# Kernel tuning notes

Measured on AMD Instinct MI355X. Metric: run time of the kernel, lower is better.

Reference implementation:

```python
import jax, jax.numpy as jnp
import numpy as np

N1 = 6000
N2 = 6000
H = 256
F_DIM = 768
G_DIM = 64
KNN = 5


def setup_inputs() -> dict:
    key = jax.random.key(0)
    ks = jax.random.split(key, 12)
    d = {
        "src_feature_0": jax.random.normal(ks[0], (N1, F_DIM), jnp.float32),
        "src_feature_1": jax.random.normal(ks[1], (N2, F_DIM), jnp.float32),
        "src_embedding_0": jax.random.normal(ks[2], (N1, H), jnp.float32),
        "src_embedding_1": jax.random.normal(ks[3], (N2, H), jnp.float32),
        "src_y_0": jax.random.randint(ks[4], (N1,), 0, 2, jnp.int64),
        "src_y_1": jax.random.randint(ks[5], (N2,), 0, 2, jnp.int64),
        "src_graphlet_0": jax.random.normal(ks[6], (N1, G_DIM), jnp.float32),
        "src_graphlet_1": jax.random.normal(ks[7], (N2, G_DIM), jnp.float32),
        # GCNConv params: lin weight [out,in] (applied as x @ W.T), bias [out]
        "gnn_weight": jax.random.normal(ks[8], (H, H), jnp.float32) / np.sqrt(H),
        "gnn_bias": jnp.zeros((H,), jnp.float32),
        # Attention combiner: Linear(H, 1)
        "attn_weight": jax.random.normal(ks[9], (1, H), jnp.float32) / np.sqrt(H),
        "attn_bias": jnp.zeros((1,), jnp.float32),
    }
    return d


def _construct_edges(emb, n_list, knn):
    """kNN cross-domain graph: cosine sim, zero within-domain blocks, row-wise topk.
    Returns (src, dst, edge_weight_indicator) with exactly N*knn candidate edges;
    edges whose masked similarity is exactly 0 get weight 0 (mirrors torch.nonzero
    dropping them)."""
    n = emb.shape[0]
    v = emb / jnp.maximum(jnp.linalg.norm(emb, axis=1, keepdims=True), 1e-12)
    adj = v @ v.T  # [N, N] dense similarity
    # zero the within-domain diagonal blocks
    dom_id = jnp.concatenate([jnp.full((m,), i, jnp.int32) for i, m in enumerate(n_list)])
    same = dom_id[:, None] == dom_id[None, :]
    adj = jnp.where(same, 0.0, adj)
    topk_val, topk_idx = jax.lax.top_k(adj, knn)  # [N, knn]
    src = jnp.repeat(jnp.arange(n, dtype=jnp.int32), knn)      # sp_row
    dst = topk_idx.reshape(-1).astype(jnp.int32)                # sp_col
    w = (topk_val.reshape(-1) != 0.0).astype(emb.dtype)         # existing-edge indicator
    return src, dst, w


def _gcn(x, src, dst, w, weight, bias):
    """PyG GCNConv with add_self_loops and symmetric normalization."""
    n = x.shape[0]
    loop = jnp.arange(n, dtype=jnp.int32)
    s = jnp.concatenate([src, loop])
    t = jnp.concatenate([dst, loop])
    ew = jnp.concatenate([w, jnp.ones((n,), x.dtype)])
    deg = jax.ops.segment_sum(ew, t, num_segments=n)
    dinv = jnp.where(deg > 0, jax.lax.rsqrt(jnp.maximum(deg, 1e-30)), 0.0)
    norm = dinv[s] * ew * dinv[t]  # [E]
    xw = x @ weight.T              # [N, H]
    msg = norm[:, None] * xw[s]    # gather + scale
    out = jax.ops.segment_sum(msg, t, num_segments=n)  # scatter-add at targets
    return out + bias


def _attention(inputs, w, b):
    stacked = jnp.stack(inputs, axis=1)                 # [N, 2, H]
    scores = stacked @ w.T + b                          # [N, 2, 1]
    weights = jax.nn.softmax(scores, axis=1)
    return jnp.sum(stacked * weights, axis=1)           # [N, H]


def _simple_mmd(x, y):
    # linear-kernel MMD: squared distance of mean embeddings
    d = jnp.mean(x, axis=0) - jnp.mean(y, axis=0)
    return jnp.sum(d * d)


def reference(src_feature_0, src_feature_1, src_embedding_0, src_embedding_1,
              src_y_0, src_y_1, src_graphlet_0, src_graphlet_1,
              gnn_weight, gnn_bias, attn_weight, attn_bias):
    n_list = [src_feature_0.shape[0], src_feature_1.shape[0]]
    emb = jnp.concatenate([src_embedding_0, src_embedding_1], axis=0)  # [N, H]
    # graph construction is under torch.no_grad
    src, dst, w = _construct_edges(jax.lax.stop_gradient(emb), n_list, KNN)
    updated = _gcn(emb, src, dst, w, gnn_weight, gnn_bias)
    updated = _attention([emb, updated], attn_weight, attn_bias)  # cross_output == 'concat'
    # src_pair_loss: pairwise MMD over domains, i != j, halved
    e0 = updated[:n_list[0]]
    e1 = updated[n_list[0]:]
    loss = (_simple_mmd(e0, e1) + _simple_mmd(e1, e0)) / 2.0
    return loss, updated
```

## Files before the change

kernel.cpp:

```cpp
#include <hip/hip_runtime.h>
#include <stdint.h>

typedef unsigned short u16;
typedef __attribute__((ext_vector_type(8))) short bf16x8;
typedef __attribute__((ext_vector_type(4))) float f32x4;
typedef __attribute__((ext_vector_type(4))) unsigned short us4;

#define ND 6000
#define NT 12000
#define HD 256
#define NCH 8
#define CHW 750
#define LDH 136

__device__ __forceinline__ float bf2f(unsigned int u) {
  u = (u & 0xffffu) << 16;
  return __builtin_bit_cast(float, u);
}
__device__ __forceinline__ u16 f2bf(float f) {
  unsigned int x = __builtin_bit_cast(unsigned int, f);
  x += 0x7fffu + ((x >> 16) & 1u);
  return (u16)(x >> 16);
}
template <int M>
__device__ __forceinline__ void tk_ins(float x, int idx, float* tv, int* ti) {
  #pragma unroll
  for (int k = 0; k < M; ++k) {
    if (x > tv[k]) { float ov = tv[k]; int oi = ti[k]; tv[k] = x; ti[k] = idx; x = ov; idx = oi; }
  }
}

__global__ __launch_bounds__(256) void k_prep(const void* __restrict__ e0, const void* __restrict__ e1,
                                              const void* __restrict__ gw, const void* __restrict__ gb,
                                              const void* __restrict__ aw, const void* __restrict__ ab,
                                              u16* __restrict__ ce, u16* __restrict__ cgwh,
                                              float* __restrict__ pgb, float* __restrict__ paw,
                                              float* __restrict__ pab, float* __restrict__ rinv,
                                              double* __restrict__ rinv64,
                                              int* __restrict__ cnt, int* __restrict__ fill,
                                              float* __restrict__ macc, int* __restrict__ flag) {
  const int b = blockIdx.x, tid = threadIdx.x;
  uint2 du = ((const uint2*)e0)[tid];
  float dv0 = bf2f(du.x), dv2 = bf2f(du.y);
  int big = (!(fabsf(dv0) <= 1024.0f)) || (!(fabsf(dv2) <= 1024.0f));
  const int isf32 = __syncthreads_or(big);
  if (b == 0 && tid == 0) flag[0] = isf32;

  if (b < 3000) {
    int i = b * 256 + tid;
    const void* src; int li;
    if (i < 384000) { src = e0; li = i; } else { src = e1; li = i - 384000; }
    us4 h;
    float f0, f1, f2, f3;
    if (isf32) {
      float4 v = ((const float4*)src)[li];
      f0 = v.x; f1 = v.y; f2 = v.z; f3 = v.w;
      h[0] = f2bf(v.x); h[1] = f2bf(v.y); h[2] = f2bf(v.z); h[3] = f2bf(v.w);
    } else {
      h = ((const us4*)src)[li];
      f0 = bf2f(h[0]); f1 = bf2f(h[1]); f2 = bf2f(h[2]); f3 = bf2f(h[3]);
    }
    *(us4*)(ce + (size_t)i * 4) = h;
    double s = (double)f0 * f0 + (double)f1 * f1 + (double)f2 * f2 + (double)f3 * f3;
    #pragma unroll
    for (int off = 32; off > 0; off >>= 1) s += __shfl_xor(s, off);
    if ((tid & 63) == 0) {
      double rd = 1.0 / fmax(sqrt(s), 1e-12);
      int node = i >> 6;
      rinv[node] = (float)rd;
      rinv64[node] = rd;
    }
    if (b < 47) {
      int k = b * 256 + tid;
      if (k < NT) { cnt[k] = 0; fill[k] = 0; }
      if (k < 512) macc[k] = 0.0f;
    }
  } else if (b < 3064) {
    int i = (b - 3000) * 256 + tid;
    us4 h;
    if (isf32) {
      float4 v = ((const float4*)gw)[i];
      h[0] = f2bf(v.x); h[1] = f2bf(v.y); h[2] = f2bf(v.z); h[3] = f2bf(v.w);
    } else {
      h = ((const us4*)gw)[i];
    }
    *(us4*)(cgwh + (size_t)i * 4) = h;
  } else {
    if (isf32) {
      pgb[tid] = ((const float*)gb)[tid];
      paw[tid] = ((const float*)aw)[tid];
      if (tid == 0) pab[0] = ((const float*)ab)[0];
    } else {
      pgb[tid] = bf2f(((const u16*)gb)[tid]);
      paw[tid] = bf2f(((const u16*)aw)[tid]);
      if (tid == 0) pab[0] = bf2f(((const u16*)ab)[0]);
    }
  }
}

__global__ __launch_bounds__(256) void k_sim(const u16* __restrict__ ce, const float* __restrict__ rinv,
                                             float* __restrict__ pval, int* __restrict__ pidx) {
  const int pass = blockIdx.z;
  const int qrow0 = pass ? ND : 0;
  const int crow0 = pass ? 0 : ND;
  const int qbase = blockIdx.x * 64;
  const int cch = blockIdx.y * CHW;
  const int cend = (cch + CHW < ND) ? cch + CHW : ND;
  const int tid = threadIdx.x, w = tid >> 6, l = tid & 63;
  const int l15 = l & 15, lq = l >> 4;

  __shared__ __align__(16) short ldsC[64 * LDH];

  int ql = qbase + w * 16 + l15; if (ql > ND - 1) ql = ND - 1;
  const u16* qh = ce + (size_t)(qrow0 + ql) * HD;
  bf16x8 afh[8];
  #pragma unroll
  for (int kk = 0; kk < 8; ++kk) afh[kk] = *(const bf16x8*)(qh + kk * 32 + lq * 8);
  const u16* C = ce + (size_t)crow0 * HD;

  unsigned int tvl[4][8];
  #pragma unroll
  for (int j = 0; j < 4; ++j)
    #pragma unroll
    for (int k = 0; k < 8; ++k) tvl[j][k] = 0u;

  for (int c0 = cch; c0 < cend; c0 += 64) {
    f32x4 acc[4];
    #pragma unroll
    for (int ct = 0; ct < 4; ++ct) acc[ct] = (f32x4){0.f, 0.f, 0.f, 0.f};
    #pragma unroll
    for (int kh = 0; kh < 2; ++kh) {
      #pragma unroll
      for (int sw = 0; sw < 4; ++sw) {
        int flat = (sw * 256 + tid) * 8;
        int r = flat >> 7, col = flat & 127;
        int cr = c0 + r; if (cr > cend - 1) cr = cend - 1;
        *(int4*)&ldsC[r * LDH + col] = *(const int4*)(C + (size_t)cr * HD + kh * 128 + col);
      }
      __syncthreads();
      #pragma unroll
      for (int ks = 0; ks < 4; ++ks) {
        #pragma unroll
        for (int ct = 0; ct < 4; ++ct) {
          bf16x8 bh = *(const bf16x8*)&ldsC[(ct * 16 + l15) * LDH + ks * 32 + lq * 8];
          acc[ct] = __builtin_amdgcn_mfma_f32_16x16x32_bf16(bh, afh[kh * 4 + ks], acc[ct], 0, 0, 0);
        }
      }
      __syncthreads();
    }
    const float* rbase = rinv + crow0 + c0 + lq * 4;
    const int lim = cend - c0;
    const int cl0 = (c0 - cch) + lq * 4;
    if (lim >= 64) {
      #pragma unroll
      for (int ct = 0; ct < 4; ++ct) {
        float4 rc = *(const float4*)(rbase + ct * 16);
        float rcv[4] = {rc.x, rc.y, rc.z, rc.w};
        #pragma unroll
        for (int r = 0; r < 4; ++r) {
          float x = acc[ct][r] * rcv[r];
          unsigned int u = __builtin_bit_cast(unsigned int, x);
          unsigned int ord = u ^ ((unsigned int)((int)u >> 31) | 0x80000000u);
          unsigned int key = (ord & 0xFFFFFC00u) | (unsigned int)(cl0 + ct * 16 + r);
          #pragma unroll
          for (int k = 0; k < 8; ++k) {
            unsigned int hi = key > tvl[r][k] ? key : tvl[r][k];
            key = key > tvl[r][k] ? tvl[r][k] : key;
            tvl[r][k] = hi;
          }
        }
      }
    } else {
      #pragma unroll
      for (int ct = 0; ct < 4; ++ct) {
        float4 rc = *(const float4*)(rbase + ct * 16);
        float rcv[4] = {rc.x, rc.y, rc.z, rc.w};
        #pragma unroll
        for (int r = 0; r < 4; ++r) {
          int cl64 = ct * 16 + lq * 4 + r;
          float x = acc[ct][r] * rcv[r];
          unsigned int u = __builtin_bit_cast(unsigned int, x);
          unsigned int ord = u ^ ((unsigned int)((int)u >> 31) | 0x80000000u);
          unsigned int key = (cl64 < lim)
              ? ((ord & 0xFFFFFC00u) | (unsigned int)(cl0 + ct * 16 + r)) : 0u;
          #pragma unroll
          for (int k = 0; k < 8; ++k) {
            unsigned int hi = key > tvl[r][k] ? key : tvl[r][k];
            key = key > tvl[r][k] ? tvl[r][k] : key;
            tvl[r][k] = hi;
          }
        }
      }
    }
  }

  unsigned int tv[8];
  #pragma unroll
  for (int k = 0; k < 8; ++k) tv[k] = tvl[0][k];
  #pragma unroll
  for (int j = 1; j < 4; ++j) {
    #pragma unroll
    for (int k = 0; k < 8; ++k) {
      unsigned int x = tvl[j][k];
      #pragma unroll
      for (int kk = 0; kk < 8; ++kk) {
        unsigned int hi = x > tv[kk] ? x : tv[kk];
        x = x > tv[kk] ? tv[kk] : x;
        tv[kk] = hi;
      }
    }
  }

  unsigned int* ldsK = (unsigned int*)ldsC;
  #pragma unroll
  for (int k = 0; k < 8; ++k) ldsK[tid * 9 + k] = tv[k];
  __syncthreads();
  if (tid < 64) {
    int qrow = qbase + tid;
    if (qrow < ND) {
      unsigned int mv[8];
      #pragma unroll
      for (int k = 0; k < 8; ++k) mv[k] = 0u;
      for (int q = 0; q < 4; ++q) {
        int src = (tid >> 4) * 64 + q * 16 + (tid & 15);
        #pragma unroll
        for (int k = 0; k < 8; ++k) {
          unsigned int x = ldsK[src * 9 + k];
          #pragma unroll
          for (int kk = 0; kk < 8; ++kk) {
            unsigned int hi = x > mv[kk] ? x : mv[kk];
            x = x > mv[kk] ? mv[kk] : x;
            mv[kk] = hi;
          }
        }
      }
      size_t base = ((size_t)(pass * ND + qrow) * NCH + blockIdx.y) * 8;
      #pragma unroll
      for (int k = 0; k < 8; ++k) {
        unsigned int key = mv[k];
        int id = -1; float f = -1e30f;
        if (key != 0u) {
          id = crow0 + cch + (int)(key & 1023u);
          unsigned int uo = (key & 0x80000000u) ? (key ^ 0x80000000u) : ~key;
          f = __builtin_bit_cast(float, uo);
        }
        pval[base + k] = f; pidx[base + k] = id;
      }
    }
  }
}

__global__ __launch_bounds__(256) void k_merge(const float* __restrict__ pval, const int* __restrict__ pidx,
                                               int* __restrict__ aIdx) {
  int n = blockIdx.x * 256 + threadIdx.x;
  if (n >= NT) return;
  int pass = (n >= ND) ? 1 : 0;
  int local = pass ? n - ND : n;
  float mv[12]; int mi[12];
  #pragma unroll
  for (int k = 0; k < 12; ++k) { mv[k] = -1e30f; mi[k] = -1; }
  for (int ch = 0; ch < NCH; ++ch) {
    size_t base = ((size_t)(pass * ND + local) * NCH + ch) * 8;
    #pragma unroll
    for (int k = 0; k < 8; ++k) {
      float x = pval[base + k]; int id = pidx[base + k];
      if (id >= 0 && x > mv[11]) tk_ins<12>(x, id, mv, mi);
    }
  }
  #pragma unroll
  for (int k = 0; k < 12; ++k) aIdx[n * 12 + k] = mi[k];
}

__global__ __launch_bounds__(256) void k_exact(const void* __restrict__ e0raw, const void* __restrict__ e1raw,
                                               const int* __restrict__ aIdx, const double* __restrict__ rinv64,
                                               const int* __restrict__ flag,
                                               int* __restrict__ edst, int* __restrict__ cnt) {
  int tid = threadIdx.x, w = tid >> 6, l = tid & 63;
  int n = blockIdx.x * 4 + w;
  const int isf32 = flag[0];
  int qloc = (n < ND) ? n : n - ND;
  const void* qb = (n < ND) ? e0raw : e1raw;
  double q0, q1, q2, q3;
  if (isf32) {
    float4 v = *(const float4*)((const float*)qb + (size_t)qloc * HD + l * 4);
    q0 = v.x; q1 = v.y; q2 = v.z; q3 = v.w;
  } else {
    us4 v = *(const us4*)((const u16*)qb + (size_t)qloc * HD + l * 4);
    q0 = bf2f(v[0]); q1 = bf2f(v[1]); q2 = bf2f(v[2]); q3 = bf2f(v[3]);
  }
  double dv[12]; int di[12];
  #pragma unroll
  for (int c = 0; c < 12; ++c) {
    int cid = aIdx[n * 12 + c];
    int cidc = (cid < 0) ? 0 : cid;
    int cloc = (cidc < ND) ? cidc : cidc - ND;
    const void* cb = (cidc < ND) ? e0raw : e1raw;
    double c0, c1, c2, c3;
    if (isf32) {
      float4 v = *(const float4*)((const float*)cb + (size_t)cloc * HD + l * 4);
      c0 = v.x; c1 = v.y; c2 = v.z; c3 = v.w;
    } else {
      us4 v = *(const us4*)((const u16*)cb + (size_t)cloc * HD + l * 4);
      c0 = bf2f(v[0]); c1 = bf2f(v[1]); c2 = bf2f(v[2]); c3 = bf2f(v[3]);
    }
    double dot = q0 * c0 + q1 * c1 + q2 * c2 + q3 * c3;
    #pragma unroll
    for (int off = 32; off > 0; off >>= 1) dot += __shfl_xor(dot, off);
    double rv = rinv64[cidc];
    dv[c] = (cid < 0) ? -1e300 : dot * rv;
    di[c] = cid;
  }
  if (l == 0) {
    double tv5[5]; int ti5[5];
    #pragma unroll
    for (int k = 0; k < 5; ++k) { tv5[k] = -1e300; ti5[k] = -1; }
    #pragma unroll
    for (int c = 0; c < 12; ++c) {
      double x = dv[c]; int id = di[c];
      #pragma unroll
      for (int k = 0; k < 5; ++k) {
        if (x > tv5[k]) { double ov = tv5[k]; int oi = ti5[k]; tv5[k] = x; ti5[k] = id; x = ov; id = oi; }
      }
    }
    #pragma unroll
    for (int k = 0; k < 5; ++k) {
      int d = (ti5[k] >= 0 && tv5[k] > 0.0) ? ti5[k] : -1;
      edst[n * 5 + k] = d;
      if (d >= 0) atomicAdd(&cnt[d], 1);
    }
  }
}

__global__ __launch_bounds__(256) void k_xw(const u16* __restrict__ ce, const u16* __restrict__ gwh,
                                            u16* __restrict__ xwb) {
  int tid = threadIdx.x, w = tid >> 6, l = tid & 63;
  int l15 = l & 15, lq = l >> 4;
  int m0 = blockIdx.x * 64 + w * 16 + l15;
  int mc = (m0 < NT) ? m0 : NT - 1;
  const u16* arow = ce + (size_t)mc * HD;
  bf16x8 afr[8];
  #pragma unroll
  for (int ks = 0; ks < 8; ++ks) afr[ks] = *(const bf16x8*)(arow + ks * 32 + lq * 8);
  int hbase = blockIdx.y * 64;
  for (int ct = 0; ct < 4; ++ct) {
    f32x4 acc = {0.f, 0.f, 0.f, 0.f};
    const u16* brow = gwh + (size_t)(hbase + ct * 16 + l15) * HD;
    #pragma unroll
    for (int ks = 0; ks < 8; ++ks) {
      bf16x8 b = *(const bf16x8*)(brow + ks * 32 + lq * 8);
      acc = __builtin_amdgcn_mfma_f32_16x16x32_bf16(afr[ks], b, acc, 0, 0, 0);
    }
    #pragma unroll
    for (int r = 0; r < 4; ++r) {
      int m = blockIdx.x * 64 + w * 16 + lq * 4 + r;
      if (m < NT) xwb[(size_t)m * HD + hbase + ct * 16 + l15] = f2bf(acc[r]);
    }
  }
}

__global__ __launch_bounds__(1024) void k_scan(const int* __restrict__ cnt,
                                               int* __restrict__ coff, float* __restrict__ dinv) {
  __shared__ int wsum[16];
  int tid = threadIdx.x;
  int lane = tid & 63, wv = tid >> 6;
  int base = tid * 12;
  bool act = base < NT;
  int v[12]; int s = 0;
  #pragma unroll
  for (int j = 0; j < 12; ++j) { v[j] = act ? cnt[base + j] : 0; s += v[j]; }
  int si = s;
  #pragma unroll
  for (int off = 1; off < 64; off <<= 1) { int t2 = __shfl_up(si, off); if (lane >= off) si += t2; }
  if (lane == 63) wsum[wv] = si;
  __syncthreads();
  if (wv == 0) {
    int x = (lane < 16) ? wsum[lane] : 0;
    #pragma unroll
    for (int off = 1; off < 16; off <<= 1) { int t2 = __shfl_up(x, off); if (lane >= off) x += t2; }
    if (lane < 16) wsum[lane] = x;
  }
  __syncthreads();
  int wpre = (wv > 0) ? wsum[wv - 1] : 0;
  int excl = wpre + si - s;
  if (act) {
    #pragma unroll
    for (int j = 0; j < 12; ++j) {
      coff[base + j] = excl;
      dinv[base + j] = 1.0f / sqrtf(1.0f + (float)v[j]);
      excl += v[j];
    }
  }
  if (tid == 0) coff[NT] = wsum[15];
}

__global__ __launch_bounds__(256) void k_fill(const int* __restrict__ edst, const int* __restrict__ coff,
                                              int* __restrict__ fill, int* __restrict__ cedge) {
  int s = blockIdx.x * 256 + threadIdx.x;
  if (s >= NT * 5) return;
  int d = edst[s];
  if (d < 0) return;
  int n = s / 5;
  int p = atomicAdd(&fill[d], 1);
  cedge[coff[d] + p] = n;
}

__global__ __launch_bounds__(256) void k_gather(const void* __restrict__ e0raw, const void* __restrict__ e1raw,
                                                const u16* __restrict__ xwb, const float* __restrict__ dinv,
                                                const int* __restrict__ coff, const int* __restrict__ cedge,
                                                const float* __restrict__ pgb, const float* __restrict__ paw,
                                                const float* __restrict__ pab, const int* __restrict__ flag,
                                                void* __restrict__ outp, float* __restrict__ macc) {
  int tid = threadIdx.x, w = tid >> 6, l = tid & 63;
  const int isf32 = flag[0];
  float4 b4 = ((const float4*)pgb)[l];
  float4 a4 = ((const float4*)paw)[l];
  float ab = pab[0];
  __shared__ float bacc[256];
  bacc[tid] = 0.0f;
  __syncthreads();
  float sum0 = 0.f, sum1 = 0.f, sum2 = 0.f, sum3 = 0.f;
  int nodeBase = blockIdx.x * 16 + w * 4;
  for (int nn = 0; nn < 4; ++nn) {
    int t = nodeBase + nn;
    float dt = dinv[t];
    int o0 = coff[t], o1 = coff[t + 1];
    float g0 = 0.f, g1 = 0.f, g2 = 0.f, g3 = 0.f;
    if (o0 < o1) {
      int sc = cedge[o0];
      for (int e = o0; e < o1; ++e) {
        int sn = (e + 1 < o1) ? cedge[e + 1] : 0;
        float ds = dinv[sc];
        us4 xv = *(const us4*)(xwb + (size_t)sc * HD + l * 4);
        g0 += ds * bf2f(xv[0]); g1 += ds * bf2f(xv[1]);
        g2 += ds * bf2f(xv[2]); g3 += ds * bf2f(xv[3]);
        sc = sn;
      }
    }
    us4 xt = *(const us4*)(xwb + (size_t)t * HD + l * 4);
    g0 = dt * g0 + dt * dt * bf2f(xt[0]) + b4.x;
    g1 = dt * g1 + dt * dt * bf2f(xt[1]) + b4.y;
    g2 = dt * g2 + dt * dt * bf2f(xt[2]) + b4.z;
    g3 = dt * g3 + dt * dt * bf2f(xt[3]) + b4.w;
    int loc = (t < ND) ? t : t - ND;
    const void* ebase = (t < ND) ? e0raw : e1raw;
    float e4_0, e4_1, e4_2, e4_3;
    if (isf32) {
      float4 ev = *(const float4*)((const float*)ebase + (size_t)loc * HD + l * 4);
      e4_0 = ev.x; e4_1 = ev.y; e4_2 = ev.z; e4_3 = ev.w;
    } else {
      us4 ue = *(const us4*)((const u16*)ebase + (size_t)loc * HD + l * 4);
      e4_0 = bf2f(ue[0]); e4_1 = bf2f(ue[1]); e4_2 = bf2f(ue[2]); e4_3 = bf2f(ue[3]);
    }
    float s0 = e4_0 * a4.x + e4_1 * a4.y + e4_2 * a4.z + e4_3 * a4.w;
    float s1 = g0 * a4.x + g1 * a4.y + g2 * a4.z + g3 * a4.w;
    #pragma unroll
    for (int off = 32; off > 0; off >>= 1) { s0 += __shfl_xor(s0, off); s1 += __shfl_xor(s1, off); }
    s0 += ab; s1 += ab;
    float m = fmaxf(s0, s1);
    float p0 = __expf(s0 - m), p1 = __expf(s1 - m);
    float iz = 1.0f / (p0 + p1);
    float w0 = p0 * iz, w1 = p1 * iz;
    float u0 = w0 * e4_0 + w1 * g0;
    float u1 = w0 * e4_1 + w1 * g1;
    float u2 = w0 * e4_2 + w1 * g2;
    float u3 = w0 * e4_3 + w1 * g3;
    size_t ob = 1 + (size_t)t * HD + l * 4;
    if (isf32) {
      float* o = (float*)outp;
      o[ob + 0] = u0; o[ob + 1] = u1; o[ob + 2] = u2; o[ob + 3] = u3;
    } else {
      u16* o = (u16*)outp;
      o[ob + 0] = f2bf(u0); o[ob + 1] = f2bf(u1); o[ob + 2] = f2bf(u2); o[ob + 3] = f2bf(u3);
    }
    sum0 += u0; sum1 += u1; sum2 += u2; sum3 += u3;
  }
  atomicAdd(&bacc[l * 4 + 0], sum0);
  atomicAdd(&bacc[l * 4 + 1], sum1);
  atomicAdd(&bacc[l * 4 + 2], sum2);
  atomicAdd(&bacc[l * 4 + 3], sum3);
  __syncthreads();
  int dom = (blockIdx.x < 375) ? 0 : 1;
  atomicAdd(&macc[dom * 256 + tid], bacc[tid]);
}

__global__ __launch_bounds__(256) void k_loss(const float* __restrict__ macc, const int* __restrict__ flag,
                                              void* __restrict__ outp) {
  int tid = threadIdx.x;
  float d = (macc[tid] - macc[256 + tid]) * (1.0f / (float)ND);
  float v = d * d;
  #pragma unroll
  for (int off = 32; off > 0; off >>= 1) v += __shfl_xor(v, off);
  __shared__ float rr[4];
  if ((tid & 63) == 0) rr[tid >> 6] = v;
  __syncthreads();
  if (tid == 0) {
    float loss = rr[0] + rr[1] + rr[2] + rr[3];
    if (flag[0]) ((float*)outp)[0] = loss;
    else ((u16*)outp)[0] = f2bf(loss);
  }
}

extern "C" void kernel_launch(void* const* d_in, const int* in_sizes, int n_in,
                              void* d_out, int out_size, void* d_ws, size_t ws_size,
                              hipStream_t stream) {
  const void* e0 = d_in[2];
  const void* e1 = d_in[3];
  const void* gw = d_in[8];
  const void* gb = d_in[9];
  const void* aw = d_in[10];
  const void* abp = d_in[11];

  float* wsf = (float*)d_ws;
  size_t o = 0;
  int*    flag  = (int*)(wsf + o); o += 4;
  u16*    ce    = (u16*)(wsf + o); o += 1536000;
  u16*    cgwh  = (u16*)(wsf + o); o += 32768;
  float*  pgb   = wsf + o; o += 256;
  float*  paw   = wsf + o; o += 256;
  float*  pab   = wsf + o; o += 8;
  double* rinv64 = (double*)(wsf + o); o += 24000;
  float*  rinv  = wsf + o; o += 12032;
  float*  pval  = wsf + o; o += 768000;
  int*    pidx  = (int*)(wsf + o); o += 768000;
  u16*    xwb   = (u16*)pval;
  int*    aIdx  = (int*)(wsf + o); o += 144000;
  int*    edst  = (int*)(wsf + o); o += 60000;
  int*    cnt   = (int*)(wsf + o); o += 12000;
  int*    fill  = (int*)(wsf + o); o += 12000;
  int*    coff  = (int*)(wsf + o); o += 12008;
  int*    cedge = (int*)(wsf + o); o += 60000;
  float*  macc  = wsf + o; o += 512;
  float*  dinv  = wsf + o; o += 12000;
  (void)in_sizes; (void)n_in; (void)out_size; (void)ws_size;

  k_prep<<<3065, 256, 0, stream>>>(e0, e1, gw, gb, aw, abp, ce, cgwh, pgb, paw, pab,
                                   rinv, rinv64, cnt, fill, macc, flag);
  k_sim<<<dim3(94, NCH, 2), 256, 0, stream>>>(ce, rinv, pval, pidx);
  k_merge<<<47, 256, 0, stream>>>(pval, pidx, aIdx);
  k_xw<<<dim3(188, 4), 256, 0, stream>>>(ce, cgwh, xwb);
  k_exact<<<3000, 256, 0, stream>>>(e0, e1, aIdx, rinv64, flag, edst, cnt);
  k_scan<<<1, 1024, 0, stream>>>(cnt, coff, dinv);
  k_fill<<<235, 256, 0, stream>>>(edst, coff, fill, cedge);
  k_gather<<<750, 256, 0, stream>>>(e0, e1, xwb, dinv, coff, cedge, pgb, paw, pab, flag, d_out, macc);
  k_loss<<<1, 256, 0, stream>>>(macc, flag, d_out);
}
```

Measured before the change: 336.0 us.

## Fuse candidate merge into exact rerank, simplify top-k keys, widen gather grid

The separate k_merge kernel is removed. k_sim now writes packed sort keys, and the new k_rank kernel extracts the top 12 candidates with a wave-wide max/ballot selection before doing the exact fp64 rerank. k_sim keeps a single per-lane top-8 list instead of four, and only keeps positive similarities, which drops the sign-flip encoding and the final in-register merge. k_gather now assigns one node per wave across 3000 blocks for more parallelism, at the cost of more LDS and global atomics. Ignoring non-positive similarities could change which edges are chosen when fewer than five positive neighbours exist.

Result: slower. 349.6 us (+4.1%).

```diff
diff --git a/kernel.cpp b/kernel.cpp
--- a/kernel.cpp
+++ b/kernel.cpp
@@ -21,13 +21,6 @@
   unsigned int x = __builtin_bit_cast(unsigned int, f);
   x += 0x7fffu + ((x >> 16) & 1u);
   return (u16)(x >> 16);
-}
-template <int M>
-__device__ __forceinline__ void tk_ins(float x, int idx, float* tv, int* ti) {
-  #pragma unroll
-  for (int k = 0; k < M; ++k) {
-    if (x > tv[k]) { float ov = tv[k]; int oi = ti[k]; tv[k] = x; ti[k] = idx; x = ov; idx = oi; }
-  }
 }
 
 __global__ __launch_bounds__(256) void k_prep(const void* __restrict__ e0, const void* __restrict__ e1,
@@ -99,7 +92,7 @@
 }
 
 __global__ __launch_bounds__(256) void k_sim(const u16* __restrict__ ce, const float* __restrict__ rinv,
-                                             float* __restrict__ pval, int* __restrict__ pidx) {
+                                             unsigned int* __restrict__ kbuf) {
   const int pass = blockIdx.z;
   const int qrow0 = pass ? ND : 0;
   const int crow0 = pass ? 0 : ND;
@@ -118,11 +111,9 @@
   for (int kk = 0; kk < 8; ++kk) afh[kk] = *(const bf16x8*)(qh + kk * 32 + lq * 8);
   const u16* C = ce + (size_t)crow0 * HD;
 
-  unsigned int tvl[4][8];
-  #pragma unroll
-  for (int j = 0; j < 4; ++j)
-    #pragma unroll
-    for (int k = 0; k < 8; ++k) tvl[j][k] = 0u;
+  unsigned int tv[8];
+  #pragma unroll
+  for (int k = 0; k < 8; ++k) tv[k] = 0u;
 
   for (int c0 = cch; c0 < cend; c0 += 64) {
     f32x4 acc[4];
@@ -160,13 +151,13 @@
         for (int r = 0; r < 4; ++r) {
           float x = acc[ct][r] * rcv[r];
           unsigned int u = __builtin_bit_cast(unsigned int, x);
-          unsigned int ord = u ^ ((unsigned int)((int)u >> 31) | 0x80000000u);
-          unsigned int key = (ord & 0xFFFFFC00u) | (unsigned int)(cl0 + ct * 16 + r);
+          unsigned int key = (x > 0.0f)
+              ? ((u & 0xFFFFFC00u) | (unsigned int)(cl0 + ct * 16 + r)) : 0u;
           #pragma unroll
           for (int k = 0; k < 8; ++k) {
-            unsigned int hi = key > tvl[r][k] ? key : tvl[r][k];
-            key = key > tvl[r][k] ? tvl[r][k] : key;
-            tvl[r][k] = hi;
+            unsigned int hi = key > tv[k] ? key : tv[k];
+            key = key > tv[k] ? tv[k] : key;
+            tv[k] = hi;
           }
         }
       }
@@ -180,33 +171,15 @@
           int cl64 = ct * 16 + lq * 4 + r;
           float x = acc[ct][r] * rcv[r];
           unsigned int u = __builtin_bit_cast(unsigned int, x);
-          unsigned int ord = u ^ ((unsigned int)((int)u >> 31) | 0x80000000u);
-          unsigned int key = (cl64 < lim)
-              ? ((ord & 0xFFFFFC00u) | (unsigned int)(cl0 + ct * 16 + r)) : 0u;
+          unsigned int key = (cl64 < lim && x > 0.0f)
+              ? ((u & 0xFFFFFC00u) | (unsigned int)(cl0 + ct * 16 + r)) : 0u;
           #pragma unroll
           for (int k = 0; k < 8; ++k) {
-            unsigned int hi = key > tvl[r][k] ? key : tvl[r][k];
-            key = key > tvl[r][k] ? tvl[r][k] : key;
-            tvl[r][k] = hi;
+            unsigned int hi = key > tv[k] ? key : tv[k];
+            key = key > tv[k] ? tv[k] : key;
+            tv[k] = hi;
           }
         }
-      }
-    }
-  }
-
-  unsigned int tv[8];
-  #pragma unroll
-  for (int k = 0; k < 8; ++k) tv[k] = tvl[0][k];
-  #pragma unroll
-  for (int j = 1; j < 4; ++j) {
-    #pragma unroll
-    for (int k = 0; k < 8; ++k) {
-      unsigned int x = tvl[j][k];
-      #pragma unroll
-      for (int kk = 0; kk < 8; ++kk) {
-        unsigned int hi = x > tv[kk] ? x : tv[kk];
-        x = x > tv[kk] ? tv[kk] : x;
-        tv[kk] = hi;
       }
     }
   }
@@ -236,48 +209,42 @@
       }
       size_t base = ((size_t)(pass * ND + qrow) * NCH + blockIdx.y) * 8;
       #pragma unroll
-      for (int k = 0; k < 8; ++k) {
-        unsigned int key = mv[k];
-        int id = -1; float f = -1e30f;
-        if (key != 0u) {
-          id = crow0 + cch + (int)(key & 1023u);
-          unsigned int uo = (key & 0x80000000u) ? (key ^ 0x80000000u) : ~key;
-          f = __builtin_bit_cast(float, uo);
-        }
-        pval[base + k] = f; pidx[base + k] = id;
-      }
-    }
-  }
-}
-
-__global__ __launch_bounds__(256) void k_merge(const float* __restrict__ pval, const int* __restrict__ pidx,
-                                               int* __restrict__ aIdx) {
-  int n = blockIdx.x * 256 + threadIdx.x;
-  if (n >= NT) return;
-  int pass = (n >= ND) ? 1 : 0;
-  int local = pass ? n - ND : n;
-  float mv[12]; int mi[12];
-  #pragma unroll
-  for (int k = 0; k < 12; ++k) { mv[k] = -1e30f; mi[k] = -1; }
-  for (int ch = 0; ch < NCH; ++ch) {
-    size_t base = ((size_t)(pass * ND + local) * NCH + ch) * 8;
-    #pragma unroll
-    for (int k = 0; k < 8; ++k) {
-      float x = pval[base + k]; int id = pidx[base + k];
-      if (id >= 0 && x > mv[11]) tk_ins<12>(x, id, mv, mi);
-    }
-  }
-  #pragma unroll
-  for (int k = 0; k < 12; ++k) aIdx[n * 12 + k] = mi[k];
-}
-
-__global__ __launch_bounds__(256) void k_exact(const void* __restrict__ e0raw, const void* __restrict__ e1raw,
-                                               const int* __restrict__ aIdx, const double* __restrict__ rinv64,
-                                               const int* __restrict__ flag,
-                                               int* __restrict__ edst, int* __restrict__ cnt) {
+      for (int k = 0; k < 8; ++k) kbuf[base + k] = mv[k];
+    }
+  }
+}
+
+__global__ __launch_bounds__(256) void k_rank(const void* __restrict__ e0raw, const void* __restrict__ e1raw,
+                                              const unsigned int* __restrict__ kbuf,
+                                              const double* __restrict__ rinv64,
+                                              const int* __restrict__ flag,
+                                              int* __restrict__ edst, int* __restrict__ cnt) {
   int tid = threadIdx.x, w = tid >> 6, l = tid & 63;
   int n = blockIdx.x * 4 + w;
   const int isf32 = flag[0];
+  int pass = (n >= ND) ? 1 : 0;
+  int crow0 = pass ? 0 : ND;
+
+  unsigned int key = kbuf[(size_t)n * 64 + l];
+  int cids[12];
+  #pragma unroll
+  for (int r = 0; r < 12; ++r) {
+    unsigned int m = key;
+    #pragma unroll
+    for (int off = 32; off > 0; off >>= 1) {
+      unsigned int o = __shfl_xor(m, off);
+      m = (o > m) ? o : m;
+    }
+    int cid = -1;
+    if (m != 0u) {
+      unsigned long long b = __ballot(key == m);
+      int wl = __ffsll(b) - 1;
+      cid = crow0 + (wl >> 3) * CHW + (int)(m & 1023u);
+      if (l == wl) key = 0u;
+    }
+    cids[r] = cid;
+  }
+
   int qloc = (n < ND) ? n : n - ND;
   const void* qb = (n < ND) ? e0raw : e1raw;
   double q0, q1, q2, q3;
@@ -288,10 +255,10 @@
     us4 v = *(const us4*)((const u16*)qb + (size_t)qloc * HD + l * 4);
     q0 = bf2f(v[0]); q1 = bf2f(v[1]); q2 = bf2f(v[2]); q3 = bf2f(v[3]);
   }
-  double dv[12]; int di[12];
+  double dv[12];
   #pragma unroll
   for (int c = 0; c < 12; ++c) {
-    int cid = aIdx[n * 12 + c];
+    int cid = cids[c];
     int cidc = (cid < 0) ? 0 : cid;
     int cloc = (cidc < ND) ? cidc : cidc - ND;
     const void* cb = (cidc < ND) ? e0raw : e1raw;
@@ -308,7 +275,6 @@
     for (int off = 32; off > 0; off >>= 1) dot += __shfl_xor(dot, off);
     double rv = rinv64[cidc];
     dv[c] = (cid < 0) ? -1e300 : dot * rv;
-    di[c] = cid;
   }
   if (l == 0) {
     double tv5[5]; int ti5[5];
@@ -316,7 +282,7 @@
     for (int k = 0; k < 5; ++k) { tv5[k] = -1e300; ti5[k] = -1; }
     #pragma unroll
     for (int c = 0; c < 12; ++c) {
-      double x = dv[c]; int id = di[c];
+      double x = dv[c]; int id = cids[c];
       #pragma unroll
       for (int k = 0; k < 5; ++k) {
         if (x > tv5[k]) { double ov = tv5[k]; int oi = ti5[k]; tv5[k] = x; ti5[k] = id; x = ov; id = oi; }
@@ -418,68 +384,63 @@
   __shared__ float bacc[256];
   bacc[tid] = 0.0f;
   __syncthreads();
-  float sum0 = 0.f, sum1 = 0.f, sum2 = 0.f, sum3 = 0.f;
-  int nodeBase = blockIdx.x * 16 + w * 4;
-  for (int nn = 0; nn < 4; ++nn) {
-    int t = nodeBase + nn;
-    float dt = dinv[t];
-    int o0 = coff[t], o1 = coff[t + 1];
-    float g0 = 0.f, g1 = 0.f, g2 = 0.f, g3 = 0.f;
-    if (o0 < o1) {
-      int sc = cedge[o0];
-      for (int e = o0; e < o1; ++e) {
-        int sn = (e + 1 < o1) ? cedge[e + 1] : 0;
-        float ds = dinv[sc];
-        us4 xv = *(const us4*)(xwb + (size_t)sc * HD + l * 4);
-        g0 += ds * bf2f(xv[0]); g1 += ds * bf2f(xv[1]);
-        g2 += ds * bf2f(xv[2]); g3 += ds * bf2f(xv[3]);
-        sc = sn;
-      }
-    }
-    us4 xt = *(const us4*)(xwb + (size_t)t * HD + l * 4);
-    g0 = dt * g0 + dt * dt * bf2f(xt[0]) + b4.x;
-    g1 = dt * g1 + dt * dt * bf2f(xt[1]) + b4.y;
-    g2 = dt * g2 + dt * dt * bf2f(xt[2]) + b4.z;
-    g3 = dt * g3 + dt * dt * bf2f(xt[3]) + b4.w;
-    int loc = (t < ND) ? t : t - ND;
-    const void* ebase = (t < ND) ? e0raw : e1raw;
-    float e4_0, e4_1, e4_2, e4_3;
-    if (isf32) {
-      float4 ev = *(const float4*)((const float*)ebase + (size_t)loc * HD + l * 4);
-      e4_0 = ev.x; e4_1 = ev.y; e4_2 = ev.z; e4_3 = ev.w;
-    } else {
-      us4 ue = *(const us4*)((const u16*)ebase + (size_t)loc * HD + l * 4);
-      e4_0 = bf2f(ue[0]); e4_1 = bf2f(ue[1]); e4_2 = bf2f(ue[2]); e4_3 = bf2f(ue[3]);
-    }
-    float s0 = e4_0 * a4.x + e4_1 * a4.y + e4_2 * a4.z + e4_3 * a4.w;
-    float s1 = g0 * a4.x + g1 * a4.y + g2 * a4.z + g3 * a4.w;
-    #pragma unroll
-    for (int off = 32; off > 0; off >>= 1) { s0 += __shfl_xor(s0, off); s1 += __shfl_xor(s1, off); }
-    s0 += ab; s1 += ab;
-    float m = fmaxf(s0, s1);
-    float p0 = __expf(s0 - m), p1 = __expf(s1 - m);
-    float iz = 1.0f / (p0 + p1);
-    float w0 = p0 * iz, w1 = p1 * iz;
-    float u0 = w0 * e4_0 + w1 * g0;
-    float u1 = w0 * e4_1 + w1 * g1;
-    float u2 = w0 * e4_2 + w1 * g2;
-    float u3 = w0 * e4_3 + w1 * g3;
-    size_t ob = 1 + (size_t)t * HD + l * 4;
-    if (isf32) {
-      float* o = (float*)outp;
-      o[ob + 0] = u0; o[ob + 1] = u1; o[ob + 2] = u2; o[ob + 3] = u3;
-    } else {
-      u16* o = (u16*)outp;
-      o[ob + 0] = f2bf(u0); o[ob + 1] = f2bf(u1); o[ob + 2] = f2bf(u2); o[ob + 3] = f2bf(u3);
-    }
-    sum0 += u0; sum1 += u1; sum2 += u2; sum3 += u3;
-  }
-  atomicAdd(&bacc[l * 4 + 0], sum0);
-  atomicAdd(&bacc[l * 4 + 1], sum1);
-  atomicAdd(&bacc[l * 4 + 2], sum2);
-  atomicAdd(&bacc[l * 4 + 3], sum3);
+  int t = blockIdx.x * 4 + w;
+  float dt = dinv[t];
+  int o0 = coff[t], o1 = coff[t + 1];
+  float g0 = 0.f, g1 = 0.f, g2 = 0.f, g3 = 0.f;
+  if (o0 < o1) {
+    int sc = cedge[o0];
+    for (int e = o0; e < o1; ++e) {
+      int sn = (e + 1 < o1) ? cedge[e + 1] : 0;
+      float ds = dinv[sc];
+      us4 xv = *(const us4*)(xwb + (size_t)sc * HD + l * 4);
+      g0 += ds * bf2f(xv[0]); g1 += ds * bf2f(xv[1]);
+      g2 += ds * bf2f(xv[2]); g3 += ds * bf2f(xv[3]);
+      sc = sn;
+    }
+  }
+  us4 xt = *(const us4*)(xwb + (size_t)t * HD + l * 4);
+  g0 = dt * g0 + dt * dt * bf2f(xt[0]) + b4.x;
+  g1 = dt * g1 + dt * dt * bf2f(xt[1]) + b4.y;
+  g2 = dt * g2 + dt * dt * bf2f(xt[2]) + b4.z;
+  g3 = dt * g3 + dt * dt * bf2f(xt[3]) + b4.w;
+  int loc = (t < ND) ? t : t - ND;
+  const void* ebase = (t < ND) ? e0raw : e1raw;
+  float e4_0, e4_1, e4_2, e4_3;
+  if (isf32) {
+    float4 ev = *(const float4*)((const float*)ebase + (size_t)loc * HD + l * 4);
+    e4_0 = ev.x; e4_1 = ev.y; e4_2 = ev.z; e4_3 = ev.w;
+  } else {
+    us4 ue = *(const us4*)((const u16*)ebase + (size_t)loc * HD + l * 4);
+    e4_0 = bf2f(ue[0]); e4_1 = bf2f(ue[1]); e4_2 = bf2f(ue[2]); e4_3 = bf2f(ue[3]);
+  }
+  float s0 = e4_0 * a4.x + e4_1 * a4.y + e4_2 * a4.z + e4_3 * a4.w;
+  float s1 = g0 * a4.x + g1 * a4.y + g2 * a4.z + g3 * a4.w;
+  #pragma unroll
+  for (int off = 32; off > 0; off >>= 1) { s0 += __shfl_xor(s0, off); s1 += __shfl_xor(s1, off); }
+  s0 += ab; s1 += ab;
+  float m = fmaxf(s0, s1);
+  float p0 = __expf(s0 - m), p1 = __expf(s1 - m);
+  float iz = 1.0f / (p0 + p1);
+  float w0 = p0 * iz, w1 = p1 * iz;
+  float u0 = w0 * e4_0 + w1 * g0;
+  float u1 = w0 * e4_1 + w1 * g1;
+  float u2 = w0 * e4_2 + w1 * g2;
+  float u3 = w0 * e4_3 + w1 * g3;
+  size_t ob = 1 + (size_t)t * HD + l * 4;
+  if (isf32) {
+    float* o = (float*)outp;
+    o[ob + 0] = u0; o[ob + 1] = u1; o[ob + 2] = u2; o[ob + 3] = u3;
+  } else {
+    u16* o = (u16*)outp;
+    o[ob + 0] = f2bf(u0); o[ob + 1] = f2bf(u1); o[ob + 2] = f2bf(u2); o[ob + 3] = f2bf(u3);
+  }
+  atomicAdd(&bacc[l * 4 + 0], u0);
+  atomicAdd(&bacc[l * 4 + 1], u1);
+  atomicAdd(&bacc[l * 4 + 2], u2);
+  atomicAdd(&bacc[l * 4 + 3], u3);
   __syncthreads();
-  int dom = (blockIdx.x < 375) ? 0 : 1;
+  int dom = (blockIdx.x < 1500) ? 0 : 1;
   atomicAdd(&macc[dom * 256 + tid], bacc[tid]);
 }
 
@@ -520,10 +481,9 @@
   float*  pab   = wsf + o; o += 8;
   double* rinv64 = (double*)(wsf + o); o += 24000;
   float*  rinv  = wsf + o; o += 12032;
-  float*  pval  = wsf + o; o += 768000;
-  int*    pidx  = (int*)(wsf + o); o += 768000;
-  u16*    xwb   = (u16*)pval;
-  int*    aIdx  = (int*)(wsf + o); o += 144000;
+  unsigned int* kbuf = (unsigned int*)(wsf + o); o += 768000;
+  o += 768000;
+  u16*    xwb   = (u16*)kbuf;
   int*    edst  = (int*)(wsf + o); o += 60000;
   int*    cnt   = (int*)(wsf + o); o += 12000;
   int*    fill  = (int*)(wsf + o); o += 12000;
@@ -535,12 +495,11 @@
 
   k_prep<<<3065, 256, 0, stream>>>(e0, e1, gw, gb, aw, abp, ce, cgwh, pgb, paw, pab,
                                    rinv, rinv64, cnt, fill, macc, flag);
-  k_sim<<<dim3(94, NCH, 2), 256, 0, stream>>>(ce, rinv, pval, pidx);
-  k_merge<<<47, 256, 0, stream>>>(pval, pidx, aIdx);
+  k_sim<<<dim3(94, NCH, 2), 256, 0, stream>>>(ce, rinv, kbuf);
+  k_rank<<<3000, 256, 0, stream>>>(e0, e1, kbuf, rinv64, flag, edst, cnt);
   k_xw<<<dim3(188, 4), 256, 0, stream>>>(ce, cgwh, xwb);
-  k_exact<<<3000, 256, 0, stream>>>(e0, e1, aIdx, rinv64, flag, edst, cnt);
   k_scan<<<1, 1024, 0, stream>>>(cnt, coff, dinv);
   k_fill<<<235, 256, 0, stream>>>(edst, coff, fill, cedge);
-  k_gather<<<750, 256, 0, stream>>>(e0, e1, xwb, dinv, coff, cedge, pgb, paw, pab, flag, d_out, macc);
+  k_gather<<<3000, 256, 0, stream>>>(e0, e1, xwb, dinv, coff, cedge, pgb, paw, pab, flag, d_out, macc);
   k_loss<<<1, 256, 0, stream>>>(macc, flag, d_out);
 }
```
